# Optimization experiments

Hardware: AMD Instinct MI355X
Metric: run time of the kernel (lower is better)

The kernel has to match this reference:

```python
import jax, jax.numpy as jnp
import numpy as np

B, N, Q, D, H = 8, 2048, 256, 1024, 16
HD = D // H


def setup_inputs() -> dict:
    key = jax.random.key(0)
    ks = jax.random.split(key, 6)
    scale = 1.0 / np.sqrt(D)
    return {
        "sources": jax.random.normal(ks[0], (B, N, D), dtype=jnp.float32),
        "queries": jax.random.normal(ks[1], (B, Q, D), dtype=jnp.float32),
        "w_in": jax.random.normal(ks[2], (3 * D, D), dtype=jnp.float32) * scale,
        "b_in": jax.random.normal(ks[3], (3 * D,), dtype=jnp.float32) * 0.02,
        "w_out": jax.random.normal(ks[4], (D, D), dtype=jnp.float32) * scale,
        "b_out": jax.random.normal(ks[5], (D,), dtype=jnp.float32) * 0.02,
    }


def reference(sources, queries, w_in, b_in, w_out, b_out):
    # torch nn.MultiheadAttention (batch_first, eval mode, no attn_mask),
    # applied per-sample with equal lengths == one batched cross-attention.
    w_q, w_k, w_v = jnp.split(w_in, 3, axis=0)   # each [D, D]
    b_q, b_k, b_v = jnp.split(b_in, 3, axis=0)
    q = queries @ w_q.T + b_q                    # [B, Q, D]
    k = sources @ w_k.T + b_k                    # [B, N, D]
    v = sources @ w_v.T + b_v                    # [B, N, D]
    q = q.reshape(B, Q, H, HD)
    k = k.reshape(B, N, H, HD)
    v = v.reshape(B, N, H, HD)
    scale = 1.0 / np.sqrt(HD).astype(np.float32)
    scores = jnp.einsum("bqhd,bkhd->bhqk", q, k) * scale  # [B, H, Q, N]
    attn = jax.nn.softmax(scores, axis=-1)
    out = jnp.einsum("bhqk,bkhd->bqhd", attn, v).reshape(B, Q, D)
    out = out @ w_out.T + b_out                  # out_proj
    return out + queries                         # residual (fix=False: no norm)
```

## Files before the change

### kernel.cpp

```cpp
#include <hip/hip_runtime.h>
#include <hip/hip_bf16.h>


typedef unsigned short u16;
typedef __attribute__((ext_vector_type(8))) short short8;
typedef __attribute__((ext_vector_type(4))) float floatx4;

static_assert(sizeof(short8) == 16, "short8 must be 16B");

__device__ __forceinline__ u16 f2bf(float f) {
  unsigned int x = __float_as_uint(f);
  x += 0x7fffu + ((x >> 16) & 1u);
  return (u16)(x >> 16);
}

__device__ __forceinline__ unsigned int cvtpk(float lo, float hi) {
  unsigned int r;
  asm("v_cvt_pk_bf16_f32 %0, %1, %2" : "=v"(r) : "v"(lo), "v"(hi));
  return r;
}

__device__ __forceinline__ void gload16(const u16* g, u16* lds) {
  __builtin_amdgcn_global_load_lds(
      (const __attribute__((address_space(1))) unsigned int*)g,
      (__attribute__((address_space(3))) unsigned int*)lds, 16, 0, 0);
}

template <int N> __device__ __forceinline__ void vmwait() {
  if constexpr (N == 0)      asm volatile("s_waitcnt vmcnt(0)" ::: "memory");
  else if constexpr (N == 2) asm volatile("s_waitcnt vmcnt(2)" ::: "memory");
  else if constexpr (N == 4) asm volatile("s_waitcnt vmcnt(4)" ::: "memory");
  else if constexpr (N == 6) asm volatile("s_waitcnt vmcnt(6)" ::: "memory");
  else if constexpr (N == 8) asm volatile("s_waitcnt vmcnt(8)" ::: "memory");
  else static_assert(N == 0, "unsupported vmcnt immediate");
}

__device__ __forceinline__ void lgkm0() {
  asm volatile("s_waitcnt lgkmcnt(0)" ::: "memory");
}

__device__ __forceinline__ void sfence() { __builtin_amdgcn_sched_barrier(0); }

__global__ __launch_bounds__(256) void f2bf_multi(
    const float* __restrict__ s, u16* __restrict__ so,
    const float* __restrict__ q, u16* __restrict__ qo,
    const float* __restrict__ wi, u16* __restrict__ wio,
    const float* __restrict__ wo, u16* __restrict__ woo) {
  int i = blockIdx.x * 256 + threadIdx.x;
  const float* in; u16* out; int idx;
  if (i < 4194304)      { in = s;  out = so;  idx = i; }
  else if (i < 4718592) { in = q;  out = qo;  idx = i - 4194304; }
  else if (i < 5505024) { in = wi; out = wio; idx = i - 4718592; }
  else if (i < 5767168) { in = wo; out = woo; idx = i - 5505024; }
  else return;
  float4 v = reinterpret_cast<const float4*>(in)[idx];
  ushort4 o;
  o.x = f2bf(v.x); o.y = f2bf(v.y); o.z = f2bf(v.z); o.w = f2bf(v.w);
  reinterpret_cast<ushort4*>(out)[idx] = o;
}

template <int MT, int NT>
__device__ __forceinline__ void gemm_core(
    const u16* __restrict__ A, int lda,
    const u16* __restrict__ Bm, int ldb, int K,
    u16* __restrict__ Alds, u16* __restrict__ Blds,
    floatx4 (&acc)[MT][NT]) {
  const int t = threadIdx.x;
  const int wave = t >> 6, lane = t & 63;
  const int rr = lane & 15, kq = lane >> 4;
  constexpr int AI = MT, BI = NT;
  constexpr int AELEMS = MT * 32 * 64;
  constexpr int BELEMS = NT * 32 * 64;

  const u16* ag[AI]; u16* al[AI];
#pragma unroll
  for (int i = 0; i < AI; ++i) {
    int s = i * 256 + t;
    int row = s >> 3, c16 = s & 7;
    ag[i] = A + (size_t)row * lda + ((c16 ^ (row & 7)) * 8);
    al[i] = Alds + (size_t)(i * 256 + wave * 64) * 8;
  }
  const u16* bg[BI]; u16* blp[BI];
#pragma unroll
  for (int i = 0; i < BI; ++i) {
    int s = i * 256 + t;
    int row = s >> 3, c16 = s & 7;
    bg[i] = Bm + (size_t)row * ldb + ((c16 ^ (row & 7)) * 8);
    blp[i] = Blds + (size_t)(i * 256 + wave * 64) * 8;
  }

  const int m0w = (wave & 1) * (MT * 16);
  const int n0w = (wave >> 1) * (NT * 16);
  int aoff[MT][2], boff[NT][2];
#pragma unroll
  for (int mi = 0; mi < MT; ++mi) {
    int row = m0w + mi * 16 + rr;
#pragma unroll
    for (int kk = 0; kk < 2; ++kk)
      aoff[mi][kk] = row * 64 + (((kk * 4 + kq) ^ (row & 7)) * 8);
  }
#pragma unroll
  for (int ni = 0; ni < NT; ++ni) {
    int row = n0w + ni * 16 + rr;
#pragma unroll
    for (int kk = 0; kk < 2; ++kk)
      boff[ni][kk] = row * 64 + (((kk * 4 + kq) ^ (row & 7)) * 8);
  }

  auto compute = [&](int bs) {
    const u16* Ab = Alds + bs * AELEMS;
    const u16* Bb = Blds + bs * BELEMS;
#pragma unroll
    for (int kk = 0; kk < 2; ++kk) {
      short8 af[MT], bfr[NT];
#pragma unroll
      for (int mi = 0; mi < MT; ++mi)
        af[mi] = *reinterpret_cast<const short8*>(Ab + aoff[mi][kk]);
#pragma unroll
      for (int ni = 0; ni < NT; ++ni)
        bfr[ni] = *reinterpret_cast<const short8*>(Bb + boff[ni][kk]);
      __builtin_amdgcn_s_setprio(1);
#pragma unroll
      for (int mi = 0; mi < MT; ++mi)
#pragma unroll
        for (int ni = 0; ni < NT; ++ni)
          acc[mi][ni] = __builtin_amdgcn_mfma_f32_16x16x32_bf16(af[mi], bfr[ni], acc[mi][ni], 0, 0, 0);
      __builtin_amdgcn_s_setprio(0);
    }
  };

  const int nt = K >> 6;

#pragma unroll
  for (int i = 0; i < AI; ++i) gload16(ag[i], al[i]);
#pragma unroll
  for (int i = 0; i < BI; ++i) gload16(bg[i], blp[i]);

  int cur = 0;
#pragma unroll 1
  for (int tt = 0; tt < nt - 1; ++tt) {
    const int nxt = cur ^ 1;
    const int koff = (tt + 1) * 64;
#pragma unroll
    for (int i = 0; i < AI; ++i) gload16(ag[i] + koff, al[i] + nxt * AELEMS);
#pragma unroll
    for (int i = 0; i < BI; ++i) gload16(bg[i] + koff, blp[i] + nxt * BELEMS);
    sfence();
    vmwait<AI + BI>();
    __builtin_amdgcn_s_barrier();
    sfence();
    compute(cur);
    sfence();
    __builtin_amdgcn_s_barrier();
    cur = nxt;
  }
  sfence();
  vmwait<0>();
  __builtin_amdgcn_s_barrier();
  sfence();
  compute(cur);
}

template <int LO>
__device__ __forceinline__ void read_a8(const u16* ab, int kcol0, int kcol1,
                                        short8 (&af)[8][2]) {
#pragma unroll
  for (int mi = 0; mi < 4; ++mi) {
    af[LO + mi][0] = *reinterpret_cast<const short8*>(ab + (LO + mi) * 1024 + kcol0);
    af[LO + mi][1] = *reinterpret_cast<const short8*>(ab + (LO + mi) * 1024 + kcol1);
  }
}

template <int LO>
__device__ __forceinline__ void read_b8(const u16* bb, int kcol0, int kcol1,
                                        short8 (&bf)[4][2]) {
#pragma unroll
  for (int ni = 0; ni < 2; ++ni) {
    bf[LO + ni][0] = *reinterpret_cast<const short8*>(bb + (LO + ni) * 1024 + kcol0);
    bf[LO + ni][1] = *reinterpret_cast<const short8*>(bb + (LO + ni) * 1024 + kcol1);
  }
}

template <int M0, int N0>
__device__ __forceinline__ void quad8(const short8 (&af)[8][2], const short8 (&bf)[4][2],
                                      floatx4 (&acc)[8][4]) {
  __builtin_amdgcn_s_setprio(1);
#pragma unroll
  for (int kk = 0; kk < 2; ++kk)
#pragma unroll
    for (int mi = 0; mi < 4; ++mi)
#pragma unroll
      for (int ni = 0; ni < 2; ++ni)
        acc[M0 + mi][N0 + ni] = __builtin_amdgcn_mfma_f32_16x16x32_bf16(
            af[M0 + mi][kk], bf[N0 + ni][kk], acc[M0 + mi][N0 + ni], 0, 0, 0);
  __builtin_amdgcn_s_setprio(0);
}

__global__ __launch_bounds__(512, 2) void gemm_proj_kv8(
    const u16* __restrict__ s_bf, const u16* __restrict__ wi_bf,
    const float* __restrict__ b_in,
    u16* __restrict__ kp, u16* __restrict__ vT) {
  __shared__ __attribute__((aligned(16))) u16 Alds[2 * 256 * 64];
  __shared__ __attribute__((aligned(16))) u16 Blds[2 * 256 * 64];

  int bid = blockIdx.y * 8 + blockIdx.x;
  int nb = (bid & 7) * 64 + (bid >> 3);
  const int by = nb >> 3, bx = nb & 7;
  const int mB = by * 256;
  const int nB = bx * 256;
  const u16* Ag = s_bf + (size_t)mB * 1024;
  const u16* Wg = wi_bf + (size_t)(1024 + nB) * 1024;
  const float* bias = b_in + 1024 + nB;

  const int t = threadIdx.x;
  const int w = t >> 6, lane = t & 63;
  const int rr = lane & 15, kq = lane >> 4;
  const int wr = w >> 2, wc = w & 3;

  const u16* ga[2][2]; const u16* gb[2][2];
#pragma unroll
  for (int h = 0; h < 2; ++h)
#pragma unroll
    for (int i = 0; i < 2; ++i) {
      int s = i * 512 + t;
      int row = h * 128 + (s >> 3), c16 = s & 7;
      ga[h][i] = Ag + (size_t)row * 1024 + ((c16 ^ (row & 7)) * 8);
      gb[h][i] = Wg + (size_t)row * 1024 + ((c16 ^ (row & 7)) * 8);
    }

#define STAGE_A8(j, h) { const int d_ = ((j) & 1) * 16384;                         \
    gload16(ga[h][0] + (size_t)(j) * 64, Alds + d_ + (h) * 8192 + w * 512);        \
    gload16(ga[h][1] + (size_t)(j) * 64, Alds + d_ + (h) * 8192 + 4096 + w * 512); }
#define STAGE_B8(j, h) { const int d_ = ((j) & 1) * 16384;                         \
    gload16(gb[h][0] + (size_t)(j) * 64, Blds + d_ + (h) * 8192 + w * 512);        \
    gload16(gb[h][1] + (size_t)(j) * 64, Blds + d_ + (h) * 8192 + 4096 + w * 512); }

  const int kcol0 = ((kq) ^ (rr & 7)) * 8;
  const int kcol1 = ((4 + kq) ^ (rr & 7)) * 8;
  const u16* abase = Alds + (wr * 128 + rr) * 64;
  const u16* bbase = Blds + (wc * 64 + rr) * 64;

  short8 af[8][2], bf[4][2];
  const floatx4 zz = {0.f, 0.f, 0.f, 0.f};
  floatx4 acc[8][4];
#pragma unroll
  for (int mi = 0; mi < 8; ++mi)
#pragma unroll
    for (int ni = 0; ni < 4; ++ni) acc[mi][ni] = zz;

  STAGE_A8(0, 0); STAGE_B8(0, 0); STAGE_A8(0, 1); STAGE_B8(0, 1);
  STAGE_A8(1, 0); STAGE_B8(1, 0);
  sfence();
  vmwait<4>();
  __builtin_amdgcn_s_barrier();
  sfence();

#pragma unroll 1
  for (int kt = 0; kt < 16; ++kt) {
    const int doff = (kt & 1) * 16384;
    const u16* ab = abase + doff;
    const u16* bb = bbase + doff;
    read_a8<0>(ab, kcol0, kcol1, af);
    read_b8<0>(bb, kcol0, kcol1, bf);
    if (kt + 1 < 16) STAGE_A8(kt + 1, 1);
    sfence();
    __builtin_amdgcn_s_barrier();
    lgkm0(); sfence();
    quad8<0, 0>(af, bf, acc);
    sfence();
    __builtin_amdgcn_s_barrier();
    sfence();
    read_a8<4>(ab, kcol0, kcol1, af);
    read_b8<2>(bb, kcol0, kcol1, bf);
    if (kt + 1 < 16) STAGE_B8(kt + 1, 1);
    sfence();
    __builtin_amdgcn_s_barrier();
    lgkm0(); sfence();
    quad8<0, 2>(af, bf, acc);
    sfence();
    __builtin_amdgcn_s_barrier();
    sfence();
    if (kt + 2 < 16) STAGE_A8(kt + 2, 0);
    sfence();
    __builtin_amdgcn_s_barrier();
    quad8<4, 0>(af, bf, acc);
    sfence();
    __builtin_amdgcn_s_barrier();
    sfence();
    if (kt + 2 < 16) { STAGE_B8(kt + 2, 0); sfence(); vmwait<4>(); }
    else             { sfence(); vmwait<0>(); }
    __builtin_amdgcn_s_barrier();
    quad8<4, 2>(af, bf, acc);
    sfence();
    __builtin_amdgcn_s_barrier();
    sfence();
  }
#undef STAGE_A8
#undef STAGE_B8

  const int r4 = kq * 4;
  const int m0w = wr * 128, n0w = wc * 64;
  if (nB < 1024) {
#pragma unroll
    for (int mi = 0; mi < 8; ++mi)
#pragma unroll
      for (int ni = 0; ni < 4; ++ni) {
        int nl = n0w + ni * 16 + rr;
        float bv = bias[nl];
#pragma unroll
        for (int r = 0; r < 4; ++r) {
          int m = mB + m0w + mi * 16 + r4 + r;
          kp[(size_t)m * 1024 + nB + nl] = f2bf(acc[mi][ni][r] + bv);
        }
      }
  } else {
#pragma unroll
    for (int mi = 0; mi < 8; ++mi)
#pragma unroll
      for (int ni = 0; ni < 4; ++ni) {
        int n2 = nB + n0w + ni * 16 + rr - 1024;
        int h = n2 >> 6, d = n2 & 63;
        float bv = bias[n0w + ni * 16 + rr];
        int m0 = mB + m0w + mi * 16 + r4;
        int b = m0 >> 11, j0 = m0 & 2047;
        ushort4 o;
        o.x = f2bf(acc[mi][ni][0] + bv);
        o.y = f2bf(acc[mi][ni][1] + bv);
        o.z = f2bf(acc[mi][ni][2] + bv);
        o.w = f2bf(acc[mi][ni][3] + bv);
        *reinterpret_cast<ushort4*>(
            vT + ((size_t)(b * 16 + h) * 64 + d) * 2048 + j0) = o;
      }
  }
}

__global__ __launch_bounds__(256, 2) void gemm_proj_q(
    const u16* __restrict__ qy_bf, const u16* __restrict__ wi_bf,
    const float* __restrict__ b_in, u16* __restrict__ qp) {
  __shared__ __attribute__((aligned(16))) u16 Alds[2 * 128 * 64];
  __shared__ __attribute__((aligned(16))) u16 Blds[2 * 128 * 64];
  const int mB = blockIdx.y * 128;
  const int nB = blockIdx.x * 128;
  const u16* A = qy_bf + (size_t)mB * 1024;
  const u16* W = wi_bf + (size_t)nB * 1024;
  const float* bias = b_in + nB;

  const floatx4 zz = {0.f, 0.f, 0.f, 0.f};
  floatx4 acc[4][4] = {{zz, zz, zz, zz}, {zz, zz, zz, zz}, {zz, zz, zz, zz}, {zz, zz, zz, zz}};
  gemm_core<4, 4>(A, 1024, W, 1024, 1024, Alds, Blds, acc);

  const int lane = threadIdx.x & 63, wave = threadIdx.x >> 6;
  const int rr = lane & 15, r4 = (lane >> 4) * 4;
  const int m0w = (wave & 1) * 64, n0w = (wave >> 1) * 64;
#pragma unroll
  for (int mi = 0; mi < 4; ++mi)
#pragma unroll
    for (int ni = 0; ni < 4; ++ni) {
      int nl = n0w + ni * 16 + rr;
      float bv = bias[nl];
#pragma unroll
      for (int r = 0; r < 4; ++r) {
        int m = mB + m0w + mi * 16 + r4 + r;
        qp[(size_t)m * 1024 + nB + nl] = f2bf((acc[mi][ni][r] + bv) * 0.125f);
      }
    }
}

__global__ __launch_bounds__(512, 4) void attn_fused(
    const u16* __restrict__ qp, const u16* __restrict__ kp,
    const u16* __restrict__ vT, u16* __restrict__ ao) {
  __shared__ __attribute__((aligned(16))) u16 Klds[2][8192];
  __shared__ __attribute__((aligned(16))) u16 Vlds[2][8192];
  __shared__ __attribute__((aligned(16))) u16 Plds[8192];

  const int bid = blockIdx.x;
  const int nb = (bid & 7) * 64 + (bid >> 3);
  const int bh = nb >> 2, qb = nb & 3;
  const int b = bh >> 4, h = bh & 15;

  const int t = threadIdx.x;
  const int w = t >> 6, lane = t & 63;
  const int rr = lane & 15, kq = lane >> 4;
  const int wk = w >> 1, wq = w & 1;
  const int wPq = w >> 2, wPd = w & 3;

  const u16* qg;
  const u16* kg[2];
  const u16* vg[2];
  {
    const u16* qbase = qp + ((size_t)(b * 256 + qb * 64)) * 1024 + h * 64;
    const u16* kbase = kp + ((size_t)b * 2048) * 1024 + h * 64;
    const u16* vbase = vT + ((size_t)bh * 64) * 2048;
    { int row = t >> 3, c8 = t & 7;
      qg = qbase + (size_t)row * 1024 + ((c8 ^ (row & 7)) * 8); }
#pragma unroll
    for (int i = 0; i < 2; ++i) {
      int s = i * 512 + t;
      int r8 = s >> 3, c8 = s & 7;
      int r16 = s >> 4, c16 = s & 15;
      kg[i] = kbase + (size_t)r8 * 1024 + ((c8 ^ (r8 & 7)) * 8);
      vg[i] = vbase + (size_t)r16 * 2048 + ((c16 ^ (r16 & 7)) * 8);
    }
  }

#define STAGE_K(j) { u16* d_ = &Klds[(j) & 1][w * 512];                 \
    gload16(kg[0] + (size_t)(j) * 131072, d_);                          \
    gload16(kg[1] + (size_t)(j) * 131072, d_ + 4096); }
#define STAGE_V(j) { u16* d_ = &Vlds[(j) & 1][w * 512];                 \
    gload16(vg[0] + (size_t)(j) * 128, d_);                             \
    gload16(vg[1] + (size_t)(j) * 128, d_ + 4096); }

  gload16(qg, Plds + w * 512);
  STAGE_K(0); STAGE_V(0); STAGE_K(1);
  sfence();
  vmwait<6>();
  __builtin_amdgcn_s_barrier();
  sfence();
  short8 qf[2][2];
#pragma unroll
  for (int ni = 0; ni < 2; ++ni) {
    int qrow = wq * 32 + ni * 16 + rr;
#pragma unroll
    for (int kc = 0; kc < 2; ++kc)
      qf[ni][kc] = *reinterpret_cast<const short8*>(
          Plds + qrow * 64 + (((kc * 4 + kq) ^ (qrow & 7)) * 8));
  }
  lgkm0(); sfence();
  vmwait<2>();
  __builtin_amdgcn_s_barrier();
  sfence();

  const short ov = (rr == 0) ? (short)0x3F80 : (short)0;
  const short8 ones = {ov, ov, ov, ov, ov, ov, ov, ov};
  const floatx4 zz = {0.f, 0.f, 0.f, 0.f};
  floatx4 oacc[2] = {zz, zz};
  floatx4 acc_l[2] = {zz, zz};

  const int pq0 = wq * 32 + rr;
  const int pkb = wk * 4 + (kq >> 1);
  const int pk4 = (kq & 1) * 4;

#pragma unroll 1
  for (int kt = 0; kt < 16; ++kt) {
    const int buf = kt & 1;
    if (kt + 1 < 16) STAGE_V(kt + 1);
    sfence();
    short8 kf[2][2];
#pragma unroll
    for (int mi = 0; mi < 2; ++mi) {
      int krow = wk * 32 + mi * 16 + rr;
#pragma unroll
      for (int kc = 0; kc < 2; ++kc)
        kf[mi][kc] = *reinterpret_cast<const short8*>(
            &Klds[buf][krow * 64 + (((kc * 4 + kq) ^ (krow & 7)) * 8)]);
    }
    lgkm0(); sfence();
    floatx4 sacc[2][2] = {{zz, zz}, {zz, zz}};
    __builtin_amdgcn_s_setprio(1);
#pragma unroll
    for (int kc = 0; kc < 2; ++kc)
#pragma unroll
      for (int mi = 0; mi < 2; ++mi)
#pragma unroll
        for (int ni = 0; ni < 2; ++ni)
          sacc[mi][ni] = __builtin_amdgcn_mfma_f32_16x16x32_bf16(
              kf[mi][kc], qf[ni][kc], sacc[mi][ni], 0, 0, 0);
    __builtin_amdgcn_s_setprio(0);
    sfence();
#pragma unroll
    for (int mi = 0; mi < 2; ++mi) {
      int kb = pkb + mi * 2;
#pragma unroll
      for (int ni = 0; ni < 2; ++ni) {
        int q = pq0 + ni * 16;
        float e0 = __expf(sacc[mi][ni][0]);
        float e1 = __expf(sacc[mi][ni][1]);
        float e2 = __expf(sacc[mi][ni][2]);
        float e3 = __expf(sacc[mi][ni][3]);
        uint2 pv;
        pv.x = cvtpk(e0, e1);
        pv.y = cvtpk(e2, e3);
        *reinterpret_cast<uint2*>(
            &Plds[q * 128 + ((kb ^ (q & 7)) << 3) + pk4]) = pv;
      }
    }
    lgkm0(); sfence();
    if (kt < 15) vmwait<4>(); else vmwait<0>();
    __builtin_amdgcn_s_barrier();
    sfence();
    short8 pa[2][4], vf[4];
#pragma unroll
    for (int mi = 0; mi < 2; ++mi) {
      int qrow = wPq * 32 + mi * 16 + rr;
#pragma unroll
      for (int kc = 0; kc < 4; ++kc)
        pa[mi][kc] = *reinterpret_cast<const short8*>(
            Plds + qrow * 128 + (((kc * 4 + kq) ^ (qrow & 7)) << 3));
    }
    {
      int drow = wPd * 16 + rr;
#pragma unroll
      for (int kc = 0; kc < 4; ++kc)
        vf[kc] = *reinterpret_cast<const short8*>(
            &Vlds[buf][drow * 128 + (((kc * 4 + kq) ^ (drow & 7)) << 3)]);
    }
    lgkm0(); sfence();
    if (kt + 2 < 16) STAGE_K(kt + 2);
    sfence();
    __builtin_amdgcn_s_setprio(1);
#pragma unroll
    for (int kc = 0; kc < 4; ++kc)
#pragma unroll
      for (int mi = 0; mi < 2; ++mi) {
        oacc[mi] = __builtin_amdgcn_mfma_f32_16x16x32_bf16(
            pa[mi][kc], vf[kc], oacc[mi], 0, 0, 0);
        acc_l[mi] = __builtin_amdgcn_mfma_f32_16x16x32_bf16(
            pa[mi][kc], ones, acc_l[mi], 0, 0, 0);
      }
    __builtin_amdgcn_s_setprio(0);
    sfence();
    if (kt + 1 < 16) {
      if (kt + 2 < 16) vmwait<4>(); else vmwait<2>();
    }
    __builtin_amdgcn_s_barrier();
    sfence();
  }
#undef STAGE_K
#undef STAGE_V

  u16* aob = ao + ((size_t)(b * 256 + qb * 64)) * 1024 + h * 64;
#pragma unroll
  for (int mi = 0; mi < 2; ++mi)
#pragma unroll
    for (int r = 0; r < 4; ++r) {
      float l = __shfl(acc_l[mi][r], lane & 48, 64);
      float inv = 1.0f / l;
      int q = wPq * 32 + mi * 16 + kq * 4 + r;
      int d = wPd * 16 + rr;
      aob[(size_t)q * 1024 + d] = f2bf(oacc[mi][r] * inv);
    }
}

__global__ __launch_bounds__(256, 2) void gemm_out(
    const u16* __restrict__ A, const u16* __restrict__ W,
    const float* __restrict__ bias, const float* __restrict__ resid,
    float* __restrict__ out) {
  __shared__ __attribute__((aligned(16))) u16 Alds[2 * 64 * 64];
  __shared__ __attribute__((aligned(16))) u16 Blds[2 * 128 * 64];
  const int mB = blockIdx.y * 64;
  const int nB = blockIdx.x * 128;
  const floatx4 zz = {0.f, 0.f, 0.f, 0.f};
  floatx4 acc[2][4] = {{zz, zz, zz, zz}, {zz, zz, zz, zz}};
  gemm_core<2, 4>(A + (size_t)mB * 1024, 1024, W + (size_t)nB * 1024, 1024, 1024,
                  Alds, Blds, acc);
  const int lane = threadIdx.x & 63, wave = threadIdx.x >> 6;
  const int rr = lane & 15, r4 = (lane >> 4) * 4;
  const int m0w = (wave & 1) * 32, n0w = (wave >> 1) * 64;
#pragma unroll
  for (int mi = 0; mi < 2; ++mi)
#pragma unroll
    for (int ni = 0; ni < 4; ++ni) {
      int n = nB + n0w + ni * 16 + rr;
      float bv = bias[n];
#pragma unroll
      for (int r = 0; r < 4; ++r) {
        int m = mB + m0w + mi * 16 + r4 + r;
        size_t idx = (size_t)m * 1024 + n;
        out[idx] = acc[mi][ni][r] + bv + resid[idx];
      }
    }
}

extern "C" void kernel_launch(void* const* d_in, const int* in_sizes, int n_in,
                              void* d_out, int out_size, void* d_ws, size_t ws_size,
                              hipStream_t stream) {
  const float* sources = (const float*)d_in[0];
  const float* queries = (const float*)d_in[1];
  const float* w_in    = (const float*)d_in[2];
  const float* b_in    = (const float*)d_in[3];
  const float* w_out   = (const float*)d_in[4];
  const float* b_out   = (const float*)d_in[5];
  float* out = (float*)d_out;

  char* ws = (char*)d_ws;
  size_t off = 0;
  auto alloc = [&](size_t elems) -> u16* {
    u16* p = (u16*)(ws + off);
    off += elems * sizeof(u16);
    off = (off + 255) & ~(size_t)255;
    return p;
  };
  u16* s_bf  = alloc((size_t)16777216);
  u16* qy_bf = alloc((size_t)2097152);
  u16* wi_bf = alloc((size_t)3145728);
  u16* wo_bf = alloc((size_t)1048576);
  u16* qp    = alloc((size_t)2097152);
  u16* kp    = alloc((size_t)16777216);
  u16* vT    = alloc((size_t)16777216);
  u16* ao    = alloc((size_t)2097152);

  f2bf_multi<<<dim3(22528), 256, 0, stream>>>(
      sources, s_bf, queries, qy_bf, w_in, wi_bf, w_out, wo_bf);

  gemm_proj_kv8<<<dim3(8, 64), 512, 0, stream>>>(s_bf, wi_bf, b_in, kp, vT);
  gemm_proj_q<<<dim3(8, 16), 256, 0, stream>>>(qy_bf, wi_bf, b_in, qp);

  attn_fused<<<dim3(512), 512, 0, stream>>>(qp, kp, vT, ao);

  gemm_out<<<dim3(8, 32), 256, 0, stream>>>(ao, wo_bf, b_out, queries, out);
}
```

Measured before the change: 267.6 us.

## Load K and V fragments directly from global into registers, dropping LDS staging

Removes the double-buffered K and V LDS tiles and their async global-to-LDS staging. Each wave now loads its K and V MFMA fragments straight from global memory into registers, prefetching the next tile's fragments after the current MFMAs run. This cuts LDS footprint and LDS read traffic, which could allow more occupancy. In exchange, K and V reads are duplicated across waves with less coalesced access, and load latency is hidden only by register-level prefetch, with no explicit vmcnt waits before the fragments are used.

```diff
diff --git a/kernel.cpp b/kernel.cpp
--- a/kernel.cpp
+++ b/kernel.cpp
@@ -369,8 +369,6 @@
 __global__ __launch_bounds__(512, 4) void attn_fused(
     const u16* __restrict__ qp, const u16* __restrict__ kp,
     const u16* __restrict__ vT, u16* __restrict__ ao) {
-  __shared__ __attribute__((aligned(16))) u16 Klds[2][8192];
-  __shared__ __attribute__((aligned(16))) u16 Vlds[2][8192];
   __shared__ __attribute__((aligned(16))) u16 Plds[8192];
 
   const int bid = blockIdx.x;
@@ -384,36 +382,29 @@
   const int wk = w >> 1, wq = w & 1;
   const int wPq = w >> 2, wPd = w & 3;
 
+  const u16* qbase = qp + ((size_t)(b * 256 + qb * 64)) * 1024 + h * 64;
+  const u16* kbase = kp + ((size_t)b * 2048) * 1024 + h * 64;
+  const u16* vbase = vT + ((size_t)bh * 64) * 2048;
+
   const u16* qg;
-  const u16* kg[2];
-  const u16* vg[2];
-  {
-    const u16* qbase = qp + ((size_t)(b * 256 + qb * 64)) * 1024 + h * 64;
-    const u16* kbase = kp + ((size_t)b * 2048) * 1024 + h * 64;
-    const u16* vbase = vT + ((size_t)bh * 64) * 2048;
-    { int row = t >> 3, c8 = t & 7;
-      qg = qbase + (size_t)row * 1024 + ((c8 ^ (row & 7)) * 8); }
-#pragma unroll
-    for (int i = 0; i < 2; ++i) {
-      int s = i * 512 + t;
-      int r8 = s >> 3, c8 = s & 7;
-      int r16 = s >> 4, c16 = s & 15;
-      kg[i] = kbase + (size_t)r8 * 1024 + ((c8 ^ (r8 & 7)) * 8);
-      vg[i] = vbase + (size_t)r16 * 2048 + ((c16 ^ (r16 & 7)) * 8);
-    }
-  }
-
-#define STAGE_K(j) { u16* d_ = &Klds[(j) & 1][w * 512];                 \
-    gload16(kg[0] + (size_t)(j) * 131072, d_);                          \
-    gload16(kg[1] + (size_t)(j) * 131072, d_ + 4096); }
-#define STAGE_V(j) { u16* d_ = &Vlds[(j) & 1][w * 512];                 \
-    gload16(vg[0] + (size_t)(j) * 128, d_);                             \
-    gload16(vg[1] + (size_t)(j) * 128, d_ + 4096); }
+  { int row = t >> 3, c8 = t & 7;
+    qg = qbase + (size_t)row * 1024 + ((c8 ^ (row & 7)) * 8); }
+
+  const u16* kfp = kbase + (size_t)(wk * 32 + rr) * 1024 + kq * 8;
+  const u16* vfp = vbase + (size_t)(wPd * 16 + rr) * 2048 + kq * 8;
 
   gload16(qg, Plds + w * 512);
-  STAGE_K(0); STAGE_V(0); STAGE_K(1);
-  sfence();
-  vmwait<6>();
+  short8 kf[2][2], vf[4];
+#pragma unroll
+  for (int mi = 0; mi < 2; ++mi)
+#pragma unroll
+    for (int kc = 0; kc < 2; ++kc)
+      kf[mi][kc] = *reinterpret_cast<const short8*>(kfp + (size_t)mi * 16384 + kc * 32);
+#pragma unroll
+  for (int kc = 0; kc < 4; ++kc)
+    vf[kc] = *reinterpret_cast<const short8*>(vfp + kc * 32);
+  sfence();
+  vmwait<8>();
   __builtin_amdgcn_s_barrier();
   sfence();
   short8 qf[2][2];
@@ -426,7 +417,6 @@
           Plds + qrow * 64 + (((kc * 4 + kq) ^ (qrow & 7)) * 8));
   }
   lgkm0(); sfence();
-  vmwait<2>();
   __builtin_amdgcn_s_barrier();
   sfence();
 
@@ -442,19 +432,6 @@
 
 #pragma unroll 1
   for (int kt = 0; kt < 16; ++kt) {
-    const int buf = kt & 1;
-    if (kt + 1 < 16) STAGE_V(kt + 1);
-    sfence();
-    short8 kf[2][2];
-#pragma unroll
-    for (int mi = 0; mi < 2; ++mi) {
-      int krow = wk * 32 + mi * 16 + rr;
-#pragma unroll
-      for (int kc = 0; kc < 2; ++kc)
-        kf[mi][kc] = *reinterpret_cast<const short8*>(
-            &Klds[buf][krow * 64 + (((kc * 4 + kq) ^ (krow & 7)) * 8)]);
-    }
-    lgkm0(); sfence();
     floatx4 sacc[2][2] = {{zz, zz}, {zz, zz}};
     __builtin_amdgcn_s_setprio(1);
 #pragma unroll
@@ -466,6 +443,14 @@
           sacc[mi][ni] = __builtin_amdgcn_mfma_f32_16x16x32_bf16(
               kf[mi][kc], qf[ni][kc], sacc[mi][ni], 0, 0, 0);
     __builtin_amdgcn_s_setprio(0);
+    if (kt + 1 < 16) {
+      const u16* kp2 = kfp + (size_t)(kt + 1) * 131072;
+#pragma unroll
+      for (int mi = 0; mi < 2; ++mi)
+#pragma unroll
+        for (int kc = 0; kc < 2; ++kc)
+          kf[mi][kc] = *reinterpret_cast<const short8*>(kp2 + (size_t)mi * 16384 + kc * 32);
+    }
     sfence();
 #pragma unroll
     for (int mi = 0; mi < 2; ++mi) {
@@ -485,10 +470,9 @@
       }
     }
     lgkm0(); sfence();
-    if (kt < 15) vmwait<4>(); else vmwait<0>();
-    __builtin_amdgcn_s_barrier();
-    sfence();
-    short8 pa[2][4], vf[4];
+    __builtin_amdgcn_s_barrier();
+    sfence();
+    short8 pa[2][4];
 #pragma unroll
     for (int mi = 0; mi < 2; ++mi) {
       int qrow = wPq * 32 + mi * 16 + rr;
@@ -497,16 +481,6 @@
         pa[mi][kc] = *reinterpret_cast<const short8*>(
             Plds + qrow * 128 + (((kc * 4 + kq) ^ (qrow & 7)) << 3));
     }
-    {
-      int drow = wPd * 16 + rr;
-#pragma unroll
-      for (int kc = 0; kc < 4; ++kc)
-        vf[kc] = *reinterpret_cast<const short8*>(
-            &Vlds[buf][drow * 128 + (((kc * 4 + kq) ^ (drow & 7)) << 3)]);
-    }
-    lgkm0(); sfence();
-    if (kt + 2 < 16) STAGE_K(kt + 2);
-    sfence();
     __builtin_amdgcn_s_setprio(1);
 #pragma unroll
     for (int kc = 0; kc < 4; ++kc)
@@ -518,15 +492,16 @@
             pa[mi][kc], ones, acc_l[mi], 0, 0, 0);
       }
     __builtin_amdgcn_s_setprio(0);
-    sfence();
     if (kt + 1 < 16) {
-      if (kt + 2 < 16) vmwait<4>(); else vmwait<2>();
-    }
-    __builtin_amdgcn_s_barrier();
-    sfence();
-  }
-#undef STAGE_K
-#undef STAGE_V
+      const u16* vp2 = vfp + (size_t)(kt + 1) * 128;
+#pragma unroll
+      for (int kc = 0; kc < 4; ++kc)
+        vf[kc] = *reinterpret_cast<const short8*>(vp2 + kc * 32);
+    }
+    sfence();
+    __builtin_amdgcn_s_barrier();
+    sfence();
+  }
 
   u16* aob = ao + ((size_t)(b * 256 + qb * 64)) * 1024 + h * 64;
 #pragma unroll
```

New measurement: 296.1 us. 1.11x slower.
